# Optimization experiments

Measured on AMD Instinct MI355X. Metric: run time of the kernel, lower is better.

## Reference

```python
import jax, jax.numpy as jnp
import numpy as np

N = 100000   # nodes
E = 1600000  # edges
D = 128      # input_dim
H = 128      # hidden_dim
O = 64       # output_dim


def setup_inputs() -> dict:
    key = jax.random.key(0)
    ks = jax.random.split(key, 8)
    x = jax.random.normal(ks[0], (N, D), dtype=jnp.float32)
    edge_index = jax.random.randint(ks[1], (2, E), 0, N, dtype=jnp.int32)
    # Glorot-ish init for weights, zeros for biases (matches GCNConv/Linear defaults in spirit)
    W1 = jax.random.normal(ks[2], (D, H), dtype=jnp.float32) / np.sqrt(D)
    b1 = jnp.zeros((H,), dtype=jnp.float32)
    W2 = jax.random.normal(ks[3], (H, H), dtype=jnp.float32) / np.sqrt(H)
    b2 = jnp.zeros((H,), dtype=jnp.float32)
    Wf = jax.random.normal(ks[4], (H, O), dtype=jnp.float32) / np.sqrt(H)
    bf = jnp.zeros((O,), dtype=jnp.float32)
    return {"x": x, "W1": W1, "b1": b1, "W2": W2, "b2": b2,
            "Wf": Wf, "bf": bf, "edge_index": edge_index}


def gcn_conv(x, W, b, src, dst):
    """GCNConv: out = D^{-1/2} (A + I) D^{-1/2} (x W) + b, edges given as (src->dst)."""
    n = x.shape[0]
    h = x @ W  # [N, H]
    loop = jnp.arange(n, dtype=src.dtype)
    s = jnp.concatenate([src, loop])  # add self-loops
    d = jnp.concatenate([dst, loop])
    deg = jax.ops.segment_sum(jnp.ones_like(s, dtype=h.dtype), d, num_segments=n)
    dinv = jnp.where(deg > 0, jax.lax.rsqrt(deg), 0.0)
    coef = dinv[s] * dinv[d]                              # [E+N]
    msg = h[s] * coef[:, None]                            # gather + scale
    out = jax.ops.segment_sum(msg, d, num_segments=n)     # scatter-add aggregate
    return out + b


def reference(x, W1, b1, W2, b2, Wf, bf, edge_index):
    src, dst = edge_index[0], edge_index[1]
    h = jax.nn.relu(gcn_conv(x, W1, b1, src, dst))
    # dropout is identity in eval mode
    h = jax.nn.relu(gcn_conv(h, W2, b2, src, dst))
    return h @ Wf + bf
```

## Files before the change

kernel.cpp:

```cpp
#include <hip/hip_runtime.h>

#define FD 128
#define SCAN_B 256
#define SCAN_T 256


__global__ void k_deg(const int* __restrict__ dst, int* __restrict__ deg,
                      int* __restrict__ rank, int E) {
  int e = blockIdx.x * blockDim.x + threadIdx.x;
  if (e < E) rank[e] = atomicAdd(&deg[dst[e]], 1);
}


__global__ __launch_bounds__(SCAN_T) void k_part(const int* __restrict__ deg,
                                                 float* __restrict__ dinv,
                                                 int* __restrict__ part, int n) {
  const int b = blockIdx.x;
  const int chunk = (n + SCAN_B - 1) / SCAN_B;
  const int lo = b * chunk;
  const int hi = min(lo + chunk, n);
  int sum = 0;
  for (int i = lo + threadIdx.x; i < hi; i += SCAN_T) {
    int d = deg[i];
    sum += d;
    dinv[i] = rsqrtf((float)(d + 1));
  }
  __shared__ int red[SCAN_T / 64];
  for (int off = 32; off > 0; off >>= 1) sum += __shfl_down(sum, off, 64);
  if ((threadIdx.x & 63) == 0) red[threadIdx.x >> 6] = sum;
  __syncthreads();
  if (threadIdx.x == 0) {
    int s = 0;
#pragma unroll
    for (int w = 0; w < SCAN_T / 64; ++w) s += red[w];
    part[b] = s;
  }
}

__global__ __launch_bounds__(SCAN_B) void k_scanpart(int* __restrict__ part,
                                                     int* __restrict__ row_ptr, int n) {
  __shared__ int s[SCAN_B];
  const int t = threadIdx.x;
  int v = part[t];
  s[t] = v;
  __syncthreads();
  for (int off = 1; off < SCAN_B; off <<= 1) {
    int u = (t >= off) ? s[t - off] : 0;
    __syncthreads();
    s[t] += u;
    __syncthreads();
  }
  part[t] = s[t] - v;
  if (t == SCAN_B - 1) row_ptr[n] = s[t];
}

__global__ __launch_bounds__(SCAN_T) void k_rowptr(const int* __restrict__ deg,
                                                   const int* __restrict__ part,
                                                   int* __restrict__ row_ptr, int n) {
  const int b = blockIdx.x;
  const int chunk = (n + SCAN_B - 1) / SCAN_B;
  const int lo = b * chunk;
  const int hi = min(lo + chunk, n);
  const int sub = (chunk + SCAN_T - 1) / SCAN_T;
  const int t = threadIdx.x;
  const int slo = min(lo + t * sub, hi);
  const int shi = min(slo + sub, hi);
  int sum = 0;
  for (int i = slo; i < shi; ++i) sum += deg[i];
  __shared__ int s[SCAN_T];
  s[t] = sum;
  __syncthreads();
  for (int off = 1; off < SCAN_T; off <<= 1) {
    int u = (t >= off) ? s[t - off] : 0;
    __syncthreads();
    s[t] += u;
    __syncthreads();
  }
  int run = part[b] + s[t] - sum;
  for (int i = slo; i < shi; ++i) {
    row_ptr[i] = run;
    run += deg[i];
  }
}


__global__ void k_fill(const int* __restrict__ src, const int* __restrict__ dst,
                       const int* __restrict__ rank, const int* __restrict__ row_ptr,
                       int* __restrict__ csr_src, int E) {
  int e = blockIdx.x * blockDim.x + threadIdx.x;
  if (e < E) {
    csr_src[row_ptr[dst[e]] + rank[e]] = src[e];
  }
}


__global__ __launch_bounds__(256) void k_gemm(const float* __restrict__ A, int lda,
                                              const float* __restrict__ W, int ldw,
                                              const float* __restrict__ bias,
                                              float* __restrict__ out, int ldo, int nrows) {
  __shared__ float Ws[64 * 64];
  __shared__ float xsT[64 * 128];
  const int t  = threadIdx.x;
  const int c0 = blockIdx.y * 64;
  const int r0 = blockIdx.x * 128;

  const int rgrp = t & 31;
  const int cgrp = t >> 5;

  float acc[4][8];
#pragma unroll
  for (int i = 0; i < 4; ++i)
#pragma unroll
    for (int j = 0; j < 8; ++j)
      acc[i][j] = bias ? bias[c0 + cgrp * 8 + j] : 0.f;

  const int rr = t & 127;
  const int hk = t >> 7;

  for (int half = 0; half < 2; ++half) {
    const int kbase = half * 64;
    __syncthreads();
    for (int i = t; i < 64 * 16; i += 256) {
      int k  = i >> 4;
      int c4 = (i & 15) << 2;
      *reinterpret_cast<float4*>(&Ws[k * 64 + c4]) =
          *reinterpret_cast<const float4*>(&W[(size_t)(kbase + k) * ldw + c0 + c4]);
    }
    {
      const int row = r0 + rr;
      const float* ap = &A[(size_t)row * lda + kbase + hk * 32];
#pragma unroll
      for (int j = 0; j < 8; ++j) {
        float4 v = make_float4(0.f, 0.f, 0.f, 0.f);
        if (row < nrows) v = *reinterpret_cast<const float4*>(ap + j * 4);
        const int kb = hk * 32 + j * 4;
        xsT[(kb + 0) * 128 + rr] = v.x;
        xsT[(kb + 1) * 128 + rr] = v.y;
        xsT[(kb + 2) * 128 + rr] = v.z;
        xsT[(kb + 3) * 128 + rr] = v.w;
      }
    }
    __syncthreads();
#pragma unroll 4
    for (int k = 0; k < 64; ++k) {
      const float4 xv = *reinterpret_cast<const float4*>(&xsT[k * 128 + rgrp * 4]);
      const float4 w0 = *reinterpret_cast<const float4*>(&Ws[k * 64 + cgrp * 8]);
      const float4 w1 = *reinterpret_cast<const float4*>(&Ws[k * 64 + cgrp * 8 + 4]);
      const float x[4] = {xv.x, xv.y, xv.z, xv.w};
      const float w[8] = {w0.x, w0.y, w0.z, w0.w, w1.x, w1.y, w1.z, w1.w};
#pragma unroll
      for (int i = 0; i < 4; ++i)
#pragma unroll
        for (int j = 0; j < 8; ++j)
          acc[i][j] += x[i] * w[j];
    }
  }

#pragma unroll
  for (int i = 0; i < 4; ++i) {
    const int row = r0 + rgrp * 4 + i;
    if (row < nrows) {
      float* o = &out[(size_t)row * ldo + c0 + cgrp * 8];
      *reinterpret_cast<float4*>(o)     = make_float4(acc[i][0], acc[i][1], acc[i][2], acc[i][3]);
      *reinterpret_cast<float4*>(o + 4) = make_float4(acc[i][4], acc[i][5], acc[i][6], acc[i][7]);
    }
  }
}


__global__ __launch_bounds__(256) void k_agg(const float* __restrict__ h,
                                             const int* __restrict__ row_ptr,
                                             const int* __restrict__ csr_src,
                                             const float* __restrict__ dinv,
                                             const float* __restrict__ bias,
                                             float* __restrict__ out, int n) {
  const int node = blockIdx.x * 4 + (threadIdx.x >> 6);
  if (node >= n) return;
  const int lane = threadIdx.x & 63;
  const int sub  = lane >> 5;
  const int c4   = (lane & 31) << 2;
  const float di = dinv[node];

  float4 acc = make_float4(0.f, 0.f, 0.f, 0.f);
  const int e0 = row_ptr[node], e1 = row_ptr[node + 1];
  int e = e0;
  for (; e + 8 <= e1; e += 8) {
    const int ia = csr_src[e     + sub];
    const int ib = csr_src[e + 2 + sub];
    const int ic = csr_src[e + 4 + sub];
    const int id = csr_src[e + 6 + sub];
    const float4 va = *reinterpret_cast<const float4*>(&h[(size_t)ia * FD + c4]);
    const float4 vb = *reinterpret_cast<const float4*>(&h[(size_t)ib * FD + c4]);
    const float4 vc = *reinterpret_cast<const float4*>(&h[(size_t)ic * FD + c4]);
    const float4 vd = *reinterpret_cast<const float4*>(&h[(size_t)id * FD + c4]);
    const float ca = dinv[ia] * di;
    const float cb = dinv[ib] * di;
    const float cc = dinv[ic] * di;
    const float cd = dinv[id] * di;
    acc.x += va.x * ca + vb.x * cb + vc.x * cc + vd.x * cd;
    acc.y += va.y * ca + vb.y * cb + vc.y * cc + vd.y * cd;
    acc.z += va.z * ca + vb.z * cb + vc.z * cc + vd.z * cd;
    acc.w += va.w * ca + vb.w * cb + vc.w * cc + vd.w * cd;
  }
  for (; e + 2 <= e1; e += 2) {
    const int i0 = csr_src[e + sub];
    const float4 v = *reinterpret_cast<const float4*>(&h[(size_t)i0 * FD + c4]);
    const float c = dinv[i0] * di;
    acc.x += v.x * c; acc.y += v.y * c; acc.z += v.z * c; acc.w += v.w * c;
  }
  if (e < e1 && sub == 0) {
    const int i0 = csr_src[e];
    const float4 v = *reinterpret_cast<const float4*>(&h[(size_t)i0 * FD + c4]);
    const float c = dinv[i0] * di;
    acc.x += v.x * c; acc.y += v.y * c; acc.z += v.z * c; acc.w += v.w * c;
  }

  acc.x += __shfl_xor(acc.x, 32);
  acc.y += __shfl_xor(acc.y, 32);
  acc.z += __shfl_xor(acc.z, 32);
  acc.w += __shfl_xor(acc.w, 32);

  const float4 hs = *reinterpret_cast<const float4*>(&h[(size_t)node * FD + c4]);
  const float4 b4 = *reinterpret_cast<const float4*>(&bias[c4]);
  float4 o;
  o.x = fmaxf(acc.x + hs.x * di * di + b4.x, 0.f);
  o.y = fmaxf(acc.y + hs.y * di * di + b4.y, 0.f);
  o.z = fmaxf(acc.z + hs.z * di * di + b4.z, 0.f);
  o.w = fmaxf(acc.w + hs.w * di * di + b4.w, 0.f);
  if (sub == 0)
    *reinterpret_cast<float4*>(&out[(size_t)node * FD + c4]) = o;
}


extern "C" void kernel_launch(void* const* d_in, const int* in_sizes, int n_in,
                              void* d_out, int out_size, void* d_ws, size_t ws_size,
                              hipStream_t stream) {
  const float* x  = (const float*)d_in[0];
  const float* W1 = (const float*)d_in[1];
  const float* b1 = (const float*)d_in[2];
  const float* W2 = (const float*)d_in[3];
  const float* b2 = (const float*)d_in[4];
  const float* Wf = (const float*)d_in[5];
  const float* bf = (const float*)d_in[6];
  const int*   ei = (const int*)d_in[7];

  const int N = in_sizes[0] / FD;
  const int E = in_sizes[7] / 2;
  const int O = in_sizes[6];
  const int* src = ei;
  const int* dst = ei + E;

  char* ws = (char*)d_ws;
  size_t off = 0;
  auto alloc = [&](size_t bytes) -> void* {
    void* p = ws + off;
    off += (bytes + 255) & ~(size_t)255;
    return p;
  };
  float* A       = (float*)alloc((size_t)N * FD * 4);
  float* B       = (float*)alloc((size_t)N * FD * 4);
  int*   deg     = (int*)  alloc((size_t)N * 4);
  float* dinv    = (float*)alloc((size_t)N * 4);
  int*   row_ptr = (int*)  alloc((size_t)(N + 1) * 4);
  int*   rank    = (int*)  alloc((size_t)E * 4);
  int*   csr_src = (int*)  alloc((size_t)E * 4);
  int*   part    = (int*)  alloc((size_t)SCAN_B * 4);

  hipMemsetAsync(deg, 0, (size_t)N * 4, stream);
  k_deg     <<<(E + 255) / 256, 256, 0, stream>>>(dst, deg, rank, E);
  k_part    <<<SCAN_B, SCAN_T, 0, stream>>>(deg, dinv, part, N);
  k_scanpart<<<1, SCAN_B, 0, stream>>>(part, row_ptr, N);
  k_rowptr  <<<SCAN_B, SCAN_T, 0, stream>>>(deg, part, row_ptr, N);
  k_fill    <<<(E + 255) / 256, 256, 0, stream>>>(src, dst, rank, row_ptr, csr_src, E);

  const int gx = (N + 127) / 128;
  k_gemm<<<dim3(gx, 2), 256, 0, stream>>>(x, FD, W1, FD, nullptr, A, FD, N);
  k_agg <<<(N + 3) / 4, 256, 0, stream>>>(A, row_ptr, csr_src, dinv, b1, B, N);
  k_gemm<<<dim3(gx, 2), 256, 0, stream>>>(B, FD, W2, FD, nullptr, A, FD, N);
  k_agg <<<(N + 3) / 4, 256, 0, stream>>>(A, row_ptr, csr_src, dinv, b2, B, N);
  k_gemm<<<dim3(gx, 1), 256, 0, stream>>>(B, FD, Wf, O, bf, (float*)d_out, O, N);
}
```

Baseline: 588.3 us.

## Replace random CSR scatter with two-pass bucketed scatter through LDS

```diff
diff --git a/kernel.cpp b/kernel.cpp
--- a/kernel.cpp
+++ b/kernel.cpp
@@ -3,6 +3,8 @@
 #define FD 128
 #define SCAN_B 256
 #define SCAN_T 256
+#define FB 4096
+#define BK 13
 
 
 __global__ void k_deg(const int* __restrict__ dst, int* __restrict__ deg,
@@ -38,7 +40,9 @@
 }
 
 __global__ __launch_bounds__(SCAN_B) void k_scanpart(int* __restrict__ part,
-                                                     int* __restrict__ row_ptr, int n) {
+                                                     int* __restrict__ row_ptr,
+                                                     int* __restrict__ cursor,
+                                                     int nb, int n) {
   __shared__ int s[SCAN_B];
   const int t = threadIdx.x;
   int v = part[t];
@@ -52,6 +56,7 @@
   }
   part[t] = s[t] - v;
   if (t == SCAN_B - 1) row_ptr[n] = s[t];
+  if (t < nb) cursor[t] = t << BK;
 }
 
 __global__ __launch_bounds__(SCAN_T) void k_rowptr(const int* __restrict__ deg,
@@ -84,13 +89,86 @@
 }
 
 
-__global__ void k_fill(const int* __restrict__ src, const int* __restrict__ dst,
-                       const int* __restrict__ rank, const int* __restrict__ row_ptr,
-                       int* __restrict__ csr_src, int E) {
-  int e = blockIdx.x * blockDim.x + threadIdx.x;
-  if (e < E) {
-    csr_src[row_ptr[dst[e]] + rank[e]] = src[e];
-  }
+__global__ __launch_bounds__(256) void k_fillA(const int* __restrict__ src,
+                                               const int* __restrict__ dst,
+                                               const int* __restrict__ rank,
+                                               const int* __restrict__ row_ptr,
+                                               int* __restrict__ cursor,
+                                               unsigned int* __restrict__ staged,
+                                               int nb, int E) {
+  __shared__ unsigned int recs[FB];
+  __shared__ unsigned short bslot[FB];
+  __shared__ int cnt[SCAN_B];
+  __shared__ int base[SCAN_B];
+  __shared__ int gbase[SCAN_B];
+  __shared__ int scn[SCAN_B];
+  const int t = threadIdx.x;
+  const int e0 = blockIdx.x * FB;
+  const int total = min(FB, E - e0);
+
+  for (int i = t; i < SCAN_B; i += 256) cnt[i] = 0;
+  __syncthreads();
+
+  unsigned int myrec[16];
+  int mybkt[16];
+#pragma unroll
+  for (int j = 0; j < 16; ++j) {
+    const int e = e0 + j * 256 + t;
+    if (e < E) {
+      const int P = row_ptr[dst[e]] + rank[e];
+      mybkt[j] = P >> BK;
+      myrec[j] = ((unsigned int)src[e] << BK) | (unsigned int)(P & ((1 << BK) - 1));
+      atomicAdd(&cnt[mybkt[j]], 1);
+    } else {
+      mybkt[j] = -1;
+    }
+  }
+  __syncthreads();
+
+  const int v = cnt[t];
+  scn[t] = v;
+  __syncthreads();
+  for (int off = 1; off < SCAN_B; off <<= 1) {
+    int u = (t >= off) ? scn[t - off] : 0;
+    __syncthreads();
+    scn[t] += u;
+    __syncthreads();
+  }
+  base[t] = scn[t] - v;
+  cnt[t] = 0;
+  __syncthreads();
+
+#pragma unroll
+  for (int j = 0; j < 16; ++j) {
+    if (mybkt[j] >= 0) {
+      const int p = base[mybkt[j]] + atomicAdd(&cnt[mybkt[j]], 1);
+      recs[p] = myrec[j];
+      bslot[p] = (unsigned short)mybkt[j];
+    }
+  }
+  __syncthreads();
+
+  if (t < nb && cnt[t] > 0) gbase[t] = atomicAdd(&cursor[t], cnt[t]);
+  __syncthreads();
+
+  for (int i = t; i < total; i += 256) {
+    const int b = bslot[i];
+    staged[gbase[b] + (i - base[b])] = recs[i];
+  }
+}
+
+__global__ __launch_bounds__(256) void k_fillB(const unsigned int* __restrict__ staged,
+                                               int* __restrict__ csr_src, int E) {
+  __shared__ int lsrc[1 << BK];
+  const int p0 = blockIdx.x << BK;
+  const int n = min(1 << BK, E - p0);
+  for (int i = threadIdx.x; i < n; i += 256) {
+    const unsigned int r = staged[p0 + i];
+    lsrc[r & ((1 << BK) - 1)] = (int)(r >> BK);
+  }
+  __syncthreads();
+  for (int i = threadIdx.x; i < n; i += 256)
+    csr_src[p0 + i] = lsrc[i];
 }
 
 
@@ -249,6 +327,7 @@
   const int O = in_sizes[6];
   const int* src = ei;
   const int* dst = ei + E;
+  const int NB = (E + (1 << BK) - 1) >> BK;
 
   char* ws = (char*)d_ws;
   size_t off = 0;
@@ -257,21 +336,24 @@
     off += (bytes + 255) & ~(size_t)255;
     return p;
   };
-  float* A       = (float*)alloc((size_t)N * FD * 4);
-  float* B       = (float*)alloc((size_t)N * FD * 4);
-  int*   deg     = (int*)  alloc((size_t)N * 4);
-  float* dinv    = (float*)alloc((size_t)N * 4);
-  int*   row_ptr = (int*)  alloc((size_t)(N + 1) * 4);
-  int*   rank    = (int*)  alloc((size_t)E * 4);
-  int*   csr_src = (int*)  alloc((size_t)E * 4);
-  int*   part    = (int*)  alloc((size_t)SCAN_B * 4);
+  float*        A       = (float*)alloc((size_t)N * FD * 4);
+  float*        B       = (float*)alloc((size_t)N * FD * 4);
+  int*          deg     = (int*)  alloc((size_t)N * 4);
+  float*        dinv    = (float*)alloc((size_t)N * 4);
+  int*          row_ptr = (int*)  alloc((size_t)(N + 1) * 4);
+  int*          rank    = (int*)  alloc((size_t)E * 4);
+  int*          csr_src = (int*)  alloc((size_t)E * 4);
+  unsigned int* staged  = (unsigned int*)alloc((size_t)E * 4);
+  int*          part    = (int*)  alloc((size_t)SCAN_B * 4);
+  int*          cursor  = (int*)  alloc((size_t)SCAN_B * 4);
 
   hipMemsetAsync(deg, 0, (size_t)N * 4, stream);
   k_deg     <<<(E + 255) / 256, 256, 0, stream>>>(dst, deg, rank, E);
   k_part    <<<SCAN_B, SCAN_T, 0, stream>>>(deg, dinv, part, N);
-  k_scanpart<<<1, SCAN_B, 0, stream>>>(part, row_ptr, N);
+  k_scanpart<<<1, SCAN_B, 0, stream>>>(part, row_ptr, cursor, NB, N);
   k_rowptr  <<<SCAN_B, SCAN_T, 0, stream>>>(deg, part, row_ptr, N);
-  k_fill    <<<(E + 255) / 256, 256, 0, stream>>>(src, dst, rank, row_ptr, csr_src, E);
+  k_fillA   <<<(E + FB - 1) / FB, 256, 0, stream>>>(src, dst, rank, row_ptr, cursor, staged, NB, E);
+  k_fillB   <<<NB, 256, 0, stream>>>(staged, csr_src, E);
 
   const int gx = (N + 127) / 128;
   k_gemm<<<dim3(gx, 2), 256, 0, stream>>>(x, FD, W1, FD, nullptr, A, FD, N);
```

Result: no change. 594.2 us (+1.0%).

## Use split-bf16 MFMA (3-pass) for dense GEMMs instead of FP32 FMA

Applied to the files above, without the earlier changes.

```diff
diff --git a/kernel.cpp b/kernel.cpp
--- a/kernel.cpp
+++ b/kernel.cpp
@@ -3,6 +3,9 @@
 #define FD 128
 #define SCAN_B 256
 #define SCAN_T 256
+
+typedef __attribute__((ext_vector_type(8))) short bf16x8;
+typedef __attribute__((ext_vector_type(4))) float f32x4;
 
 
 __global__ void k_deg(const int* __restrict__ dst, int* __restrict__ deg,
@@ -94,75 +97,88 @@
 }
 
 
+__device__ __forceinline__ void split_bf16(float x, short& hi, short& lo) {
+  unsigned u = __float_as_uint(x);
+  unsigned short h = (unsigned short)((u + 0x7fffu + ((u >> 16) & 1u)) >> 16);
+  float hf = __uint_as_float((unsigned)h << 16);
+  unsigned ul = __float_as_uint(x - hf);
+  hi = (short)h;
+  lo = (short)((ul + 0x7fffu + ((ul >> 16) & 1u)) >> 16);
+}
+
 __global__ __launch_bounds__(256) void k_gemm(const float* __restrict__ A, int lda,
                                               const float* __restrict__ W, int ldw,
                                               const float* __restrict__ bias,
                                               float* __restrict__ out, int ldo, int nrows) {
-  __shared__ float Ws[64 * 64];
-  __shared__ float xsT[64 * 128];
+  __shared__ short xhi[64][136], xlo[64][136];
+  __shared__ short whi[64][136], wlo[64][136];
   const int t  = threadIdx.x;
+  const int r0 = blockIdx.x * 64;
   const int c0 = blockIdx.y * 64;
-  const int r0 = blockIdx.x * 128;
-
-  const int rgrp = t & 31;
-  const int cgrp = t >> 5;
-
-  float acc[4][8];
-#pragma unroll
-  for (int i = 0; i < 4; ++i)
-#pragma unroll
-    for (int j = 0; j < 8; ++j)
-      acc[i][j] = bias ? bias[c0 + cgrp * 8 + j] : 0.f;
-
-  const int rr = t & 127;
-  const int hk = t >> 7;
-
-  for (int half = 0; half < 2; ++half) {
-    const int kbase = half * 64;
-    __syncthreads();
-    for (int i = t; i < 64 * 16; i += 256) {
-      int k  = i >> 4;
-      int c4 = (i & 15) << 2;
-      *reinterpret_cast<float4*>(&Ws[k * 64 + c4]) =
-          *reinterpret_cast<const float4*>(&W[(size_t)(kbase + k) * ldw + c0 + c4]);
-    }
-    {
-      const int row = r0 + rr;
-      const float* ap = &A[(size_t)row * lda + kbase + hk * 32];
-#pragma unroll
-      for (int j = 0; j < 8; ++j) {
-        float4 v = make_float4(0.f, 0.f, 0.f, 0.f);
-        if (row < nrows) v = *reinterpret_cast<const float4*>(ap + j * 4);
-        const int kb = hk * 32 + j * 4;
-        xsT[(kb + 0) * 128 + rr] = v.x;
-        xsT[(kb + 1) * 128 + rr] = v.y;
-        xsT[(kb + 2) * 128 + rr] = v.z;
-        xsT[(kb + 3) * 128 + rr] = v.w;
-      }
-    }
-    __syncthreads();
-#pragma unroll 4
-    for (int k = 0; k < 64; ++k) {
-      const float4 xv = *reinterpret_cast<const float4*>(&xsT[k * 128 + rgrp * 4]);
-      const float4 w0 = *reinterpret_cast<const float4*>(&Ws[k * 64 + cgrp * 8]);
-      const float4 w1 = *reinterpret_cast<const float4*>(&Ws[k * 64 + cgrp * 8 + 4]);
-      const float x[4] = {xv.x, xv.y, xv.z, xv.w};
-      const float w[8] = {w0.x, w0.y, w0.z, w0.w, w1.x, w1.y, w1.z, w1.w};
-#pragma unroll
-      for (int i = 0; i < 4; ++i)
-#pragma unroll
-        for (int j = 0; j < 8; ++j)
-          acc[i][j] += x[i] * w[j];
-    }
-  }
-
-#pragma unroll
-  for (int i = 0; i < 4; ++i) {
-    const int row = r0 + rgrp * 4 + i;
-    if (row < nrows) {
-      float* o = &out[(size_t)row * ldo + c0 + cgrp * 8];
-      *reinterpret_cast<float4*>(o)     = make_float4(acc[i][0], acc[i][1], acc[i][2], acc[i][3]);
-      *reinterpret_cast<float4*>(o + 4) = make_float4(acc[i][4], acc[i][5], acc[i][6], acc[i][7]);
+
+  {
+    const int row  = t >> 2;
+    const int kb   = (t & 3) * 32;
+    const int grow = r0 + row;
+    const float* ap = &A[(size_t)grow * lda + kb];
+#pragma unroll
+    for (int j = 0; j < 8; ++j) {
+      float4 v = make_float4(0.f, 0.f, 0.f, 0.f);
+      if (grow < nrows) v = *reinterpret_cast<const float4*>(ap + 4 * j);
+      short4 h4, l4;
+      split_bf16(v.x, h4.x, l4.x);
+      split_bf16(v.y, h4.y, l4.y);
+      split_bf16(v.z, h4.z, l4.z);
+      split_bf16(v.w, h4.w, l4.w);
+      *reinterpret_cast<short4*>(&xhi[row][kb + 4 * j]) = h4;
+      *reinterpret_cast<short4*>(&xlo[row][kb + 4 * j]) = l4;
+    }
+  }
+  {
+    const int k  = t >> 1;
+    const int cb = (t & 1) * 32;
+    const float* wp = &W[(size_t)k * ldw + c0 + cb];
+#pragma unroll
+    for (int j = 0; j < 8; ++j) {
+      float4 v = *reinterpret_cast<const float4*>(wp + 4 * j);
+      short h, l;
+      split_bf16(v.x, h, l); whi[cb + 4 * j + 0][k] = h; wlo[cb + 4 * j + 0][k] = l;
+      split_bf16(v.y, h, l); whi[cb + 4 * j + 1][k] = h; wlo[cb + 4 * j + 1][k] = l;
+      split_bf16(v.z, h, l); whi[cb + 4 * j + 2][k] = h; wlo[cb + 4 * j + 2][k] = l;
+      split_bf16(v.w, h, l); whi[cb + 4 * j + 3][k] = h; wlo[cb + 4 * j + 3][k] = l;
+    }
+  }
+  __syncthreads();
+
+  const int w  = t >> 6;
+  const int l  = t & 63;
+  const int lr = l & 15;
+  const int lk = l >> 4;
+
+  f32x4 acc[4] = {};
+#pragma unroll
+  for (int kc = 0; kc < 4; ++kc) {
+    const int kb = kc * 32 + lk * 8;
+    const bf16x8 ah = *reinterpret_cast<const bf16x8*>(&xhi[w * 16 + lr][kb]);
+    const bf16x8 al = *reinterpret_cast<const bf16x8*>(&xlo[w * 16 + lr][kb]);
+#pragma unroll
+    for (int ct = 0; ct < 4; ++ct) {
+      const bf16x8 bh = *reinterpret_cast<const bf16x8*>(&whi[ct * 16 + lr][kb]);
+      const bf16x8 bl = *reinterpret_cast<const bf16x8*>(&wlo[ct * 16 + lr][kb]);
+      acc[ct] = __builtin_amdgcn_mfma_f32_16x16x32_bf16(ah, bh, acc[ct], 0, 0, 0);
+      acc[ct] = __builtin_amdgcn_mfma_f32_16x16x32_bf16(ah, bl, acc[ct], 0, 0, 0);
+      acc[ct] = __builtin_amdgcn_mfma_f32_16x16x32_bf16(al, bh, acc[ct], 0, 0, 0);
+    }
+  }
+
+#pragma unroll
+  for (int ct = 0; ct < 4; ++ct) {
+    const int col = c0 + ct * 16 + lr;
+    const float b = bias ? bias[col] : 0.f;
+#pragma unroll
+    for (int r = 0; r < 4; ++r) {
+      const int row = r0 + w * 16 + lk * 4 + r;
+      if (row < nrows) out[(size_t)row * ldo + col] = acc[ct][r] + b;
     }
   }
 }
@@ -273,7 +289,7 @@
   k_rowptr  <<<SCAN_B, SCAN_T, 0, stream>>>(deg, part, row_ptr, N);
   k_fill    <<<(E + 255) / 256, 256, 0, stream>>>(src, dst, rank, row_ptr, csr_src, E);
 
-  const int gx = (N + 127) / 128;
+  const int gx = (N + 63) / 64;
   k_gemm<<<dim3(gx, 2), 256, 0, stream>>>(x, FD, W1, FD, nullptr, A, FD, N);
   k_agg <<<(N + 3) / 4, 256, 0, stream>>>(A, row_ptr, csr_src, dinv, b1, B, N);
   k_gemm<<<dim3(gx, 2), 256, 0, stream>>>(B, FD, W2, FD, nullptr, A, FD, N);
```

Result: slower. 602.3 us (+2.4%).
